# Optimization experiments

Measured on AMD Instinct MI355X. Metric: run time of the kernel, lower is better.

## Reference

```python
import jax, jax.numpy as jnp
import numpy as np
import math

B, L, D, P = 2, 2048, 256, 32
PI = math.pi


def _layernorm(x, g, b, eps=1e-5):
    m = x.mean(-1, keepdims=True)
    v = x.var(-1, keepdims=True)
    return (x - m) / jnp.sqrt(v + eps) * g + b


def setup_inputs() -> dict:
    key = jax.random.key(0)
    ks = jax.random.split(key, 16)
    sd = 1.0 / math.sqrt(D)
    f32 = jnp.float32
    inp = {
        "x": jax.random.normal(ks[0], (B, L, D), f32),
        # key_encoder: Linear(D, P)
        "key_W": jax.random.normal(ks[1], (D, P), f32) * sd,
        "key_b": jnp.zeros((P,), f32),
        # value_encoder: Linear(D, D)
        "val_W": jax.random.normal(ks[2], (D, D), f32) * sd,
        "val_b": jnp.zeros((D,), f32),
        # refiner: LayerNorm(D), Linear(D, 2D), GELU, Linear(2D, D)
        "ln1_g": jnp.ones((D,), f32),
        "ln1_b": jnp.zeros((D,), f32),
        "W1": jax.random.normal(ks[3], (D, 2 * D), f32) * sd,
        "b1": jnp.zeros((2 * D,), f32),
        "W2": jax.random.normal(ks[4], (2 * D, D), f32) * (1.0 / math.sqrt(2 * D)),
        "b2": jnp.zeros((D,), f32),
        # to_out: LayerNorm(D), Linear(D, D)
        "ln2_g": jnp.ones((D,), f32),
        "ln2_b": jnp.zeros((D,), f32),
        "Wo": jax.random.normal(ks[5], (D, D), f32) * sd,
        "bo": jnp.zeros((D,), f32),
    }
    return inp


def reference(x, key_W, key_b, val_W, val_b, ln1_g, ln1_b, W1, b1, W2, b2,
              ln2_g, ln2_b, Wo, bo):
    # key phases in (-pi, pi); phasor exp(i*theta) handled as (cos, sin)
    phases = jnp.tanh(x @ key_W + key_b) * PI          # (B, L, P)
    values = x @ val_W + val_b                          # (B, L, D)

    cos_p = jnp.cos(phases)
    sin_p = jnp.sin(phases)
    # torch.roll(shifts=1, dims=1) then zero the first position -> shift right, row 0 = 0
    zrow = jnp.zeros_like(cos_p[:, :1])
    cos_s = jnp.concatenate([zrow, cos_p[:, :-1]], axis=1)
    sin_s = jnp.concatenate([zrow, sin_p[:, :-1]], axis=1)

    # odd positions hold values
    vmask = (jnp.arange(L) % 2 == 1).astype(x.dtype)    # (L,)
    mv = values * vmask[None, :, None]                  # (B, L, D)

    # bind: outer product phasor (P) x value (D); real/imag parts
    bound_re = cos_s[..., None] * mv[:, :, None, :]     # (B, L, P, D)
    bound_im = sin_s[..., None] * mv[:, :, None, :]
    mem_re = jnp.cumsum(bound_re, axis=1)
    mem_im = jnp.cumsum(bound_im, axis=1)

    # retrieve: Re[ memory * exp(-i*theta) ] summed over phases
    retrieved = (jnp.einsum('blpd,blp->bld', mem_re, cos_p)
                 + jnp.einsum('blpd,blp->bld', mem_im, sin_p))

    valid = jnp.maximum(jnp.cumsum(vmask), 1.0)         # (L,)
    retrieved = retrieved / (jnp.sqrt(valid)[None, :, None] * math.sqrt(P))

    h = _layernorm(retrieved, ln1_g, ln1_b)
    h = jax.nn.gelu(h @ W1 + b1, approximate=False)
    refined = h @ W2 + b2
    out = x + (_layernorm(refined, ln2_g, ln2_b) @ Wo + bo)
    return out
```

## Files before the change

kernel.cpp:

```cpp
#include <hip/hip_runtime.h>
#include <math.h>

#define BB 2
#define LL 2048
#define DD 256
#define PP 32
#define NC 64
#define PI_F 3.14159265358979323846f

typedef __attribute__((ext_vector_type(8))) short bf16x8;
typedef __attribute__((ext_vector_type(4))) float f32x4;
typedef unsigned short ushort_t;
typedef unsigned int uint_t;

__device__ inline ushort_t f2bf(float x) {
    uint_t u = __float_as_uint(x);
    uint_t r = (u + 0x7fffu + ((u >> 16) & 1u)) >> 16;
    return (ushort_t)r;
}

__device__ inline int swzc(int row, int col) {
    return (col & ~63) | ((((col >> 3) & 7) ^ (row & 7)) << 3);
}
__device__ inline int swze(int row, int col) {
    return (col & ~63) | (col & 7) | ((((col >> 3) & 7) ^ (row & 7)) << 3);
}

__global__ __launch_bounds__(256) void prep_key_kernel(
    const float* __restrict__ W1, const float* __restrict__ W2,
    const float* __restrict__ Wo, const float* __restrict__ valW,
    const float* __restrict__ x, const float* __restrict__ key_W,
    const float* __restrict__ key_b,
    ushort_t* __restrict__ W1t, ushort_t* __restrict__ W2t,
    ushort_t* __restrict__ Wot, ushort_t* __restrict__ valWt,
    float2* __restrict__ ph)
{
    const int bid = blockIdx.x;
    const int t = threadIdx.x;
    if (bid < 96) {
        __shared__ float T[64][65];
        const float* W; ushort_t* Wt; int K, N, tile;
        if (bid < 32)      { W = W1;   Wt = W1t;   K = 256; N = 512; tile = bid; }
        else if (bid < 64) { W = W2;   Wt = W2t;   K = 512; N = 256; tile = bid - 32; }
        else if (bid < 80) { W = Wo;   Wt = Wot;   K = 256; N = 256; tile = bid - 64; }
        else               { W = valW; Wt = valWt; K = 256; N = 256; tile = bid - 80; }
        const int ntiles = N / 64;
        const int k0 = (tile / ntiles) * 64, n0 = (tile % ntiles) * 64;
        {
            const int rr = t >> 2, cb = (t & 3) * 16;
            #pragma unroll
            for (int i = 0; i < 16; i += 4) {
                const float4 v = *(const float4*)&W[(k0 + rr) * N + n0 + cb + i];
                T[rr][cb + i + 0] = v.x; T[rr][cb + i + 1] = v.y;
                T[rr][cb + i + 2] = v.z; T[rr][cb + i + 3] = v.w;
            }
        }
        __syncthreads();
        {
            const int n = t >> 2, kb = (t & 3) * 16;
            #pragma unroll
            for (int i = 0; i < 16; ++i)
                Wt[(n0 + n) * K + k0 + kb + i] = f2bf(T[kb + i][n]);
        }
    } else {
        __shared__ ushort_t xt[16][264];
        __shared__ ushort_t kwT[32][264];
        __shared__ float rbuf[4][2][16][17];
        const int row0 = (bid - 96) * 16;
        {
            const int l = t >> 4, cb = (t & 15) * 16;
            const float* src = &x[(long)(row0 + l) * DD + cb];
            ushort_t tmp[16];
            #pragma unroll
            for (int i = 0; i < 4; ++i) {
                const float4 v = *(const float4*)&src[i * 4];
                tmp[i*4+0] = f2bf(v.x); tmp[i*4+1] = f2bf(v.y);
                tmp[i*4+2] = f2bf(v.z); tmp[i*4+3] = f2bf(v.w);
            }
            *(uint4*)&xt[l][cb]     = *(uint4*)&tmp[0];
            *(uint4*)&xt[l][cb + 8] = *(uint4*)&tmp[8];
        }
        {
            #pragma unroll
            for (int i = 0; i < 8; ++i) {
                const int idx4 = i * 256 + t;
                const int k = idx4 >> 3, pc = (idx4 & 7) * 4;
                const float4 v = *(const float4*)&key_W[k * 32 + pc];
                kwT[pc + 0][k] = f2bf(v.x);
                kwT[pc + 1][k] = f2bf(v.y);
                kwT[pc + 2][k] = f2bf(v.z);
                kwT[pc + 3][k] = f2bf(v.w);
            }
        }
        __syncthreads();
        const int wv = t >> 6, lane = t & 63;
        const int qd = lane >> 4, mc = lane & 15;
        f32x4 acc0 = {0.f,0.f,0.f,0.f}, acc1 = {0.f,0.f,0.f,0.f};
        #pragma unroll
        for (int ks = 0; ks < 2; ++ks) {
            const int ko = wv * 64 + ks * 32 + qd * 8;
            const bf16x8 a  = *(const bf16x8*)&xt[mc][ko];
            const bf16x8 b0 = *(const bf16x8*)&kwT[mc][ko];
            const bf16x8 b1 = *(const bf16x8*)&kwT[16 + mc][ko];
            acc0 = __builtin_amdgcn_mfma_f32_16x16x32_bf16(a, b0, acc0, 0, 0, 0);
            acc1 = __builtin_amdgcn_mfma_f32_16x16x32_bf16(a, b1, acc1, 0, 0, 0);
        }
        #pragma unroll
        for (int r = 0; r < 4; ++r) {
            rbuf[wv][0][qd * 4 + r][mc] = acc0[r];
            rbuf[wv][1][qd * 4 + r][mc] = acc1[r];
        }
        __syncthreads();
        #pragma unroll
        for (int rep = 0; rep < 2; ++rep) {
            const int idx = rep * 256 + t;
            const int p = idx & 31, l = idx >> 5;
            const int nf = p >> 4, mcol = p & 15;
            float a = key_b[p] + rbuf[0][nf][l][mcol] + rbuf[1][nf][l][mcol]
                    + rbuf[2][nf][l][mcol] + rbuf[3][nf][l][mcol];
            a = tanhf(a) * PI_F;
            float sn, cs;
            sincosf(a, &sn, &cs);
            ph[(long)(row0 + l) * PP + p] = make_float2(cs, sn);
        }
    }
}

__global__ __launch_bounds__(256) void valbind_kernel(
    const float* __restrict__ x, const float2* __restrict__ ph,
    const ushort_t* __restrict__ valWt, const float* __restrict__ val_b,
    ushort_t* __restrict__ VoddT, float* __restrict__ Mt)
{
    __shared__ ushort_t xsb[16][264];
    __shared__ ushort_t VdT[64][40];
    __shared__ ushort_t phsT[64][40];
    __shared__ float    Ms[64][68];

    const int tid = threadIdx.x;
    const int bid = blockIdx.x;
    const int b  = bid >> 8;
    const int c  = (bid >> 2) & 63;
    const int dq = bid & 3;
    const int base = b * LL;
    const int r0 = 32 * c;

    {
        const int j = tid >> 4, cb = (tid & 15) * 16;
        const float* src = &x[(long)(base + r0 + 2 * j + 1) * DD + cb];
        ushort_t tmp[16];
        #pragma unroll
        for (int i = 0; i < 4; ++i) {
            const float4 v = *(const float4*)&src[i * 4];
            tmp[i*4+0] = f2bf(v.x); tmp[i*4+1] = f2bf(v.y);
            tmp[i*4+2] = f2bf(v.z); tmp[i*4+3] = f2bf(v.w);
        }
        *(uint4*)&xsb[j][cb]     = *(uint4*)&tmp[0];
        *(uint4*)&xsb[j][cb + 8] = *(uint4*)&tmp[8];
    }
    {
        const int j = tid >> 4, qb = (tid & 15) * 4;
        const float4 v = *(const float4*)((const float*)ph +
                              (long)(base + r0 + 2 * j) * 64 + qb);
        phsT[qb + 0][j] = f2bf(v.x);
        phsT[qb + 1][j] = f2bf(v.y);
        phsT[qb + 2][j] = f2bf(v.z);
        phsT[qb + 3][j] = f2bf(v.w);
    }
    for (int e = tid; e < 64 * 16; e += 256) {
        phsT[e >> 4][16 + (e & 15)] = 0;
        VdT[e >> 4][16 + (e & 15)] = 0;
    }
    __syncthreads();

    const int wv = tid >> 6, lane = tid & 63;
    const int qd = lane >> 4, mc = lane & 15;

    f32x4 va = {0.f,0.f,0.f,0.f};
    const int dloc = wv * 16 + mc;
    const int ng = dq * 64 + dloc;
    const ushort_t* B0 = &valWt[(long)ng * 256];
    #pragma unroll
    for (int ks = 0; ks < 8; ++ks) {
        const bf16x8 a  = *(const bf16x8*)&xsb[mc][ks * 32 + qd * 8];
        const bf16x8 b0 = *(const bf16x8*)&B0[ks * 32 + qd * 8];
        va = __builtin_amdgcn_mfma_f32_16x16x32_bf16(a, b0, va, 0, 0, 0);
    }
    {
        const float bb = val_b[ng];
        #pragma unroll
        for (int r = 0; r < 4; ++r)
            VdT[dloc][qd * 4 + r] = f2bf(va[r] + bb);
    }
    __syncthreads();

    const bf16x8 a2 = *(const bf16x8*)&phsT[wv * 16 + mc][qd * 8];
    f32x4 macc[4];
    #pragma unroll
    for (int nf = 0; nf < 4; ++nf) {
        f32x4 z = {0.f,0.f,0.f,0.f};
        const bf16x8 b2 = *(const bf16x8*)&VdT[nf * 16 + mc][qd * 8];
        macc[nf] = __builtin_amdgcn_mfma_f32_16x16x32_bf16(a2, b2, z, 0, 0, 0);
    }
    #pragma unroll
    for (int nf = 0; nf < 4; ++nf) {
        #pragma unroll
        for (int r = 0; r < 4; ++r)
            Ms[nf * 16 + mc][wv * 16 + qd * 4 + r] = macc[nf][r];
    }
    __syncthreads();

    {
        float* dst = &Mt[((long)(b * NC + c) * 256 + dq * 64) * 64];
        #pragma unroll
        for (int p = 0; p < 4; ++p) {
            const int idx4 = p * 256 + tid;
            const int dl = idx4 >> 4, q4 = (idx4 & 15) * 4;
            *(float4*)&dst[dl * 64 + q4] = *(const float4*)&Ms[dl][q4];
        }
    }
    if (tid < 64) {
        ushort_t* vd = &VoddT[((long)(b * NC + c) * 256 + dq * 64 + tid) * 16];
        *(uint4*)&vd[0] = *(const uint4*)&VdT[tid][0];
        *(uint4*)&vd[8] = *(const uint4*)&VdT[tid][8];
    }
}

__global__ __launch_bounds__(256) void prefix_kernel(
    const float* __restrict__ M, ushort_t* __restrict__ Mpre_b)
{
    __shared__ float segsum[4][64];
    const int tid = threadIdx.x;
    const int b  = blockIdx.x >> 8;
    const int cg = blockIdx.x & 255;
    const int col = cg * 64 + (tid & 63);
    const int seg = tid >> 6;
    const long base = (long)b * NC * 16384 + col;

    float v[16], s = 0.f;
    #pragma unroll
    for (int i = 0; i < 16; ++i) {
        v[i] = M[base + (long)(seg * 16 + i) * 16384];
        s += v[i];
    }
    segsum[seg][tid & 63] = s;
    __syncthreads();
    float run = 0.f;
    #pragma unroll
    for (int sg = 0; sg < 3; ++sg)
        if (sg < seg) run += segsum[sg][tid & 63];
    #pragma unroll
    for (int i = 0; i < 16; ++i) {
        const long a = base + (long)(seg * 16 + i) * 16384;
        Mpre_b[a] = f2bf(run);
        run += v[i];
    }
}

__global__ __launch_bounds__(512) void retrieve_mlp_kernel(
    const float* __restrict__ ph, const ushort_t* __restrict__ Mpre_b,
    const ushort_t* __restrict__ VoddT,
    const float* __restrict__ ln1_g, const float* __restrict__ ln1_b,
    const ushort_t* __restrict__ W1t, const float* __restrict__ b1,
    const ushort_t* __restrict__ W2t, const float* __restrict__ b2,
    const float* __restrict__ ln2_g, const float* __restrict__ ln2_b,
    const ushort_t* __restrict__ Wot, const float* __restrict__ bo,
    const float* __restrict__ x, float* __restrict__ out)
{
    __shared__ ushort_t Bs_v[256][32];
    __shared__ ushort_t As_ph[16][64];
    __shared__ ushort_t Bs_sh[16][64];
    __shared__ ushort_t As_p[16][40];
    __shared__ float    refct[16][264];
    __shared__ ushort_t rhat_s[16][256];
    __shared__ ushort_t h_s[16][512];
    __shared__ ushort_t shT[16][256];

    const int tid = threadIdx.x;
    const int b = blockIdx.x >> 7;
    const int c = (blockIdx.x >> 1) & 63;
    const int h = blockIdx.x & 1;
    const int l0g = 32 * c + 16 * h;
    const long rowbase = (long)b * LL + l0g;

    if (tid < 256) {
        const int r = tid >> 4, q4 = (tid & 15) * 4;
        const int c4 = swze(r, q4);
        const float4 vv = *(const float4*)((const float*)ph + (rowbase + r) * 64 + q4);
        ushort_t t0[4] = {f2bf(vv.x), f2bf(vv.y), f2bf(vv.z), f2bf(vv.w)};
        *(uint2*)&As_ph[r][c4] = *(uint2*)t0;
        const float4 w = *(const float4*)((const float*)ph +
                             ((long)b * LL + 32 * c + 2 * r) * 64 + q4);
        ushort_t t1[4] = {f2bf(w.x), f2bf(w.y), f2bf(w.z), f2bf(w.w)};
        *(uint2*)&Bs_sh[r][c4] = *(uint2*)t1;
    }
    {
        const ushort_t* src = &VoddT[(long)(b * NC + c) * 4096];
        const int rw = tid >> 1, cch = tid & 1;
        *(uint4*)&Bs_v[rw][8 * (cch ^ (rw & 3))] = *(const uint4*)&src[tid * 8];
        *(uint4*)&Bs_v[rw][8 * ((2 + cch) ^ (rw & 3))] = make_uint4(0, 0, 0, 0);
        if (tid < 256) As_p[tid >> 4][16 + (tid & 15)] = 0;
    }
    __syncthreads();

    const int wv = tid >> 6, lane = tid & 63;
    const int qd = lane >> 4, mc = lane & 15;
    const int m7 = mc & 7;

    {
        f32x4 sacc = {0.f, 0.f, 0.f, 0.f};
        #pragma unroll
        for (int ks = 0; ks < 2; ++ks) {
            const int lc = 8 * ((ks * 4 + qd) ^ m7);
            const bf16x8 a  = *(const bf16x8*)&As_ph[mc][lc];
            const bf16x8 bb = *(const bf16x8*)&Bs_sh[mc][lc];
            sacc = __builtin_amdgcn_mfma_f32_16x16x32_bf16(a, bb, sacc, 0, 0, 0);
        }
        if (wv == 0) {
            #pragma unroll
            for (int r = 0; r < 4; ++r) {
                const int l = qd * 4 + r;
                As_p[l][mc] = (2 * mc + 1 <= 16 * h + l) ? f2bf(sacc[r])
                                                         : (ushort_t)0;
            }
        }
    }

    const ushort_t* msrc = &Mpre_b[(long)(b * NC + c) * 16384];
    f32x4 acc[2];
    #pragma unroll
    for (int i = 0; i < 2; ++i) acc[i] = (f32x4){0.f, 0.f, 0.f, 0.f};
    #pragma unroll
    for (int i = 0; i < 2; ++i) {
        const int d0 = wv * 32 + i * 16;
        #pragma unroll
        for (int ks = 0; ks < 2; ++ks) {
            const int lc = 8 * ((ks * 4 + qd) ^ m7);
            const bf16x8 a  = *(const bf16x8*)&As_ph[mc][lc];
            const bf16x8 bb = *(const bf16x8*)&msrc[(long)(d0 + mc) * 64 + ks * 32 + qd * 8];
            acc[i] = __builtin_amdgcn_mfma_f32_16x16x32_bf16(a, bb, acc[i], 0, 0, 0);
        }
    }
    __syncthreads();

    {
        const bf16x8 a2 = *(const bf16x8*)&As_p[mc][qd * 8];
        #pragma unroll
        for (int i = 0; i < 2; ++i) {
            const int d0 = wv * 32 + i * 16;
            const bf16x8 b2 = *(const bf16x8*)&Bs_v[d0 + mc][8 * (qd ^ (mc & 3))];
            acc[i] = __builtin_amdgcn_mfma_f32_16x16x32_bf16(a2, b2, acc[i], 0, 0, 0);
        }
    }

    #pragma unroll
    for (int r = 0; r < 4; ++r) {
        const int l = qd * 4 + r;
        int va = (l0g + l + 1) >> 1; if (va < 1) va = 1;
        const float sc = 0.17677669529663687f * rsqrtf((float)va);
        #pragma unroll
        for (int i = 0; i < 2; ++i)
            refct[l][wv * 32 + i * 16 + mc] = acc[i][r] * sc;
    }
    __syncthreads();

    {
        const int row = tid >> 5, cg = (tid & 31) * 8;
        float s = 0.f, sq = 0.f;
        #pragma unroll
        for (int i = 0; i < 8; ++i) {
            const float v = refct[row][cg + i];
            s += v; sq += v * v;
        }
        s += __shfl_xor(s, 1, 32);  sq += __shfl_xor(sq, 1, 32);
        s += __shfl_xor(s, 2, 32);  sq += __shfl_xor(sq, 2, 32);
        s += __shfl_xor(s, 4, 32);  sq += __shfl_xor(sq, 4, 32);
        s += __shfl_xor(s, 8, 32);  sq += __shfl_xor(sq, 8, 32);
        s += __shfl_xor(s, 16, 32); sq += __shfl_xor(sq, 16, 32);
        const float m = s * (1.f / 256.f);
        const float inv = rsqrtf(sq * (1.f / 256.f) - m * m + 1e-5f);
        ushort_t o16[8];
        #pragma unroll
        for (int i = 0; i < 8; ++i) {
            const int cc = cg + i;
            o16[i] = f2bf((refct[row][cc] - m) * inv * ln1_g[cc] + ln1_b[cc]);
        }
        *(uint4*)&rhat_s[row][swzc(row, cg)] = *(uint4*)&o16[0];
    }
    __syncthreads();

    #pragma unroll
    for (int nh = 0; nh < 2; ++nh) {
        f32x4 acc1[2];
        acc1[0] = (f32x4){0.f,0.f,0.f,0.f};
        acc1[1] = (f32x4){0.f,0.f,0.f,0.f};
        const long nb0 = (long)(nh * 256 + wv * 32 + mc) * 256;
        const long nb1 = (long)(nh * 256 + wv * 32 + 16 + mc) * 256;
        #pragma unroll
        for (int k0 = 0; k0 < 256; k0 += 64) {
            #pragma unroll
            for (int ks = 0; ks < 2; ++ks) {
                const int kk = k0 + ks * 32 + qd * 8;
                const int lc = 8 * ((ks * 4 + qd) ^ m7);
                const bf16x8 a  = *(const bf16x8*)&rhat_s[mc][k0 + lc];
                const bf16x8 b0 = *(const bf16x8*)&W1t[nb0 + kk];
                const bf16x8 b1v = *(const bf16x8*)&W1t[nb1 + kk];
                acc1[0] = __builtin_amdgcn_mfma_f32_16x16x32_bf16(a, b0, acc1[0], 0, 0, 0);
                acc1[1] = __builtin_amdgcn_mfma_f32_16x16x32_bf16(a, b1v, acc1[1], 0, 0, 0);
            }
        }
        #pragma unroll
        for (int nf = 0; nf < 2; ++nf) {
            const int n = nh * 256 + wv * 32 + nf * 16 + mc;
            const float bb = b1[n];
            #pragma unroll
            for (int r = 0; r < 4; ++r) {
                float v = acc1[nf][r] + bb;
                v = 0.5f * v * (1.f + erff(v * 0.70710678118654752f));
                const int rw = qd * 4 + r;
                h_s[rw][swze(rw, n)] = f2bf(v);
            }
        }
    }
    __syncthreads();

    f32x4 acc2[2];
    acc2[0] = (f32x4){0.f,0.f,0.f,0.f};
    acc2[1] = (f32x4){0.f,0.f,0.f,0.f};
    {
        const long nb0 = (long)(wv * 32 + mc) * 512;
        const long nb1 = (long)(wv * 32 + 16 + mc) * 512;
        #pragma unroll
        for (int k0 = 0; k0 < 512; k0 += 64) {
            #pragma unroll
            for (int ks = 0; ks < 2; ++ks) {
                const int kk = k0 + ks * 32 + qd * 8;
                const int lc = 8 * ((ks * 4 + qd) ^ m7);
                const bf16x8 a  = *(const bf16x8*)&h_s[mc][k0 + lc];
                const bf16x8 b0 = *(const bf16x8*)&W2t[nb0 + kk];
                const bf16x8 b1v = *(const bf16x8*)&W2t[nb1 + kk];
                acc2[0] = __builtin_amdgcn_mfma_f32_16x16x32_bf16(a, b0, acc2[0], 0, 0, 0);
                acc2[1] = __builtin_amdgcn_mfma_f32_16x16x32_bf16(a, b1v, acc2[1], 0, 0, 0);
            }
        }
    }
    #pragma unroll
    for (int nf = 0; nf < 2; ++nf) {
        const int n = wv * 32 + nf * 16 + mc;
        const float bb = b2[n];
        #pragma unroll
        for (int r = 0; r < 4; ++r)
            refct[qd * 4 + r][n] = acc2[nf][r] + bb;
    }
    __syncthreads();

    {
        const int row = tid >> 5, cg = (tid & 31) * 8;
        float s = 0.f, sq = 0.f;
        #pragma unroll
        for (int i = 0; i < 8; ++i) {
            const float v = refct[row][cg + i];
            s += v; sq += v * v;
        }
        s += __shfl_xor(s, 1, 32);  sq += __shfl_xor(sq, 1, 32);
        s += __shfl_xor(s, 2, 32);  sq += __shfl_xor(sq, 2, 32);
        s += __shfl_xor(s, 4, 32);  sq += __shfl_xor(sq, 4, 32);
        s += __shfl_xor(s, 8, 32);  sq += __shfl_xor(sq, 8, 32);
        s += __shfl_xor(s, 16, 32); sq += __shfl_xor(sq, 16, 32);
        const float m = s * (1.f / 256.f);
        const float inv = rsqrtf(sq * (1.f / 256.f) - m * m + 1e-5f);
        ushort_t o16[8];
        #pragma unroll
        for (int i = 0; i < 8; ++i) {
            const int cc = cg + i;
            o16[i] = f2bf((refct[row][cc] - m) * inv * ln2_g[cc] + ln2_b[cc]);
        }
        *(uint4*)&shT[row][swzc(row, cg)] = *(uint4*)&o16[0];
    }
    __syncthreads();

    f32x4 acc3[2];
    acc3[0] = (f32x4){0.f,0.f,0.f,0.f};
    acc3[1] = (f32x4){0.f,0.f,0.f,0.f};
    {
        const long nb0 = (long)(wv * 32 + mc) * 256;
        const long nb1 = (long)(wv * 32 + 16 + mc) * 256;
        #pragma unroll
        for (int k0 = 0; k0 < 256; k0 += 64) {
            #pragma unroll
            for (int ks = 0; ks < 2; ++ks) {
                const int kk = k0 + ks * 32 + qd * 8;
                const int lc = 8 * ((ks * 4 + qd) ^ m7);
                const bf16x8 a  = *(const bf16x8*)&shT[mc][k0 + lc];
                const bf16x8 b0 = *(const bf16x8*)&Wot[nb0 + kk];
                const bf16x8 b1v = *(const bf16x8*)&Wot[nb1 + kk];
                acc3[0] = __builtin_amdgcn_mfma_f32_16x16x32_bf16(a, b0, acc3[0], 0, 0, 0);
                acc3[1] = __builtin_amdgcn_mfma_f32_16x16x32_bf16(a, b1v, acc3[1], 0, 0, 0);
            }
        }
    }
    #pragma unroll
    for (int nf = 0; nf < 2; ++nf) {
        const int n = wv * 32 + nf * 16 + mc;
        const float bb = bo[n];
        #pragma unroll
        for (int r = 0; r < 4; ++r) {
            const long row = rowbase + qd * 4 + r;
            out[row * DD + n] = acc3[nf][r] + bb + x[row * DD + n];
        }
    }
}

extern "C" void kernel_launch(void* const* d_in, const int* in_sizes, int n_in,
                              void* d_out, int out_size, void* d_ws, size_t ws_size,
                              hipStream_t stream)
{
    const float* x     = (const float*)d_in[0];
    const float* key_W = (const float*)d_in[1];
    const float* key_b = (const float*)d_in[2];
    const float* val_W = (const float*)d_in[3];
    const float* val_b = (const float*)d_in[4];
    const float* ln1_g = (const float*)d_in[5];
    const float* ln1_b = (const float*)d_in[6];
    const float* W1    = (const float*)d_in[7];
    const float* b1    = (const float*)d_in[8];
    const float* W2    = (const float*)d_in[9];
    const float* b2    = (const float*)d_in[10];
    const float* ln2_g = (const float*)d_in[11];
    const float* ln2_b = (const float*)d_in[12];
    const float* Wo    = (const float*)d_in[13];
    const float* bo    = (const float*)d_in[14];
    float* outp = (float*)d_out;

    float* ws = (float*)d_ws;
    float*  ph      = ws;
    float*  Mt      = ws + 262144;
    ushort_t* Mpre_b = (ushort_t*)(Mt + 2097152);
    ushort_t* VoddT  = Mpre_b + 2097152;
    ushort_t* rhat_b = VoddT + 524288;
    ushort_t* W1t   = rhat_b + 1048576;
    ushort_t* W2t   = W1t + 131072;
    ushort_t* Wot   = W2t + 131072;
    ushort_t* valWt = Wot + 65536;

    prep_key_kernel<<<352, 256, 0, stream>>>(W1, W2, Wo, val_W, x, key_W, key_b,
                                             W1t, W2t, Wot, valWt, (float2*)ph);
    valbind_kernel<<<512, 256, 0, stream>>>(x, (const float2*)ph, valWt, val_b,
                                            VoddT, Mt);
    prefix_kernel<<<512, 256, 0, stream>>>(Mt, Mpre_b);
    retrieve_mlp_kernel<<<256, 512, 0, stream>>>(ph, Mpre_b, VoddT, ln1_g, ln1_b,
                                                 W1t, b1, W2t, b2, ln2_g, ln2_b,
                                                 Wot, bo, x, outp);
}
```

Baseline: 124.2 us.

## Double block to 1024 threads and stage weight tiles through LDS

The retrieve/MLP kernel now runs 16 waves per block, and each wave computes one 16-column tile instead of two. The memory prefix tile and the W1/W2/Wo weight slices are loaded cooperatively into a swizzled shared buffer, replacing per-wave direct global fragment loads. This aims to coalesce weight reads and raise the number of waves in flight. In exchange it adds two block-wide barriers per K-step, and with a 16-row M tile the weights are reused little, so the barriers may dominate.

```diff
diff --git a/kernel.cpp b/kernel.cpp
--- a/kernel.cpp
+++ b/kernel.cpp
@@ -256,7 +256,7 @@
     }
 }
 
-__global__ __launch_bounds__(512) void retrieve_mlp_kernel(
+__global__ __launch_bounds__(1024) void retrieve_mlp_kernel(
     const float* __restrict__ ph, const ushort_t* __restrict__ Mpre_b,
     const ushort_t* __restrict__ VoddT,
     const float* __restrict__ ln1_g, const float* __restrict__ ln1_b,
@@ -266,6 +266,7 @@
     const ushort_t* __restrict__ Wot, const float* __restrict__ bo,
     const float* __restrict__ x, float* __restrict__ out)
 {
+    __shared__ ushort_t Bs_m[256][64];
     __shared__ ushort_t Bs_v[256][32];
     __shared__ ushort_t As_ph[16][64];
     __shared__ ushort_t Bs_sh[16][64];
@@ -282,6 +283,15 @@
     const int l0g = 32 * c + 16 * h;
     const long rowbase = (long)b * LL + l0g;
 
+    {
+        const ushort_t* src = &Mpre_b[(long)(b * NC + c) * 16384];
+        #pragma unroll
+        for (int p = 0; p < 2; ++p) {
+            const int idx8 = p * 1024 + tid;
+            const int d = idx8 >> 3, ch = idx8 & 7;
+            *(uint4*)&Bs_m[d][8 * (ch ^ (d & 7))] = *(const uint4*)&src[idx8 * 8];
+        }
+    }
     if (tid < 256) {
         const int r = tid >> 4, q4 = (tid & 15) * 4;
         const int c4 = swze(r, q4);
@@ -293,18 +303,22 @@
         ushort_t t1[4] = {f2bf(w.x), f2bf(w.y), f2bf(w.z), f2bf(w.w)};
         *(uint2*)&Bs_sh[r][c4] = *(uint2*)t1;
     }
-    {
+    if (tid < 512) {
         const ushort_t* src = &VoddT[(long)(b * NC + c) * 4096];
         const int rw = tid >> 1, cch = tid & 1;
         *(uint4*)&Bs_v[rw][8 * (cch ^ (rw & 3))] = *(const uint4*)&src[tid * 8];
         *(uint4*)&Bs_v[rw][8 * ((2 + cch) ^ (rw & 3))] = make_uint4(0, 0, 0, 0);
-        if (tid < 256) As_p[tid >> 4][16 + (tid & 15)] = 0;
+    }
+    if (tid >= 512 && tid < 768) {
+        const int e = tid - 512;
+        As_p[e >> 4][16 + (e & 15)] = 0;
     }
     __syncthreads();
 
     const int wv = tid >> 6, lane = tid & 63;
     const int qd = lane >> 4, mc = lane & 15;
     const int m7 = mc & 7;
+    const int d0 = wv * 16;
 
     {
         f32x4 sacc = {0.f, 0.f, 0.f, 0.f};
@@ -325,31 +339,20 @@
         }
     }
 
-    const ushort_t* msrc = &Mpre_b[(long)(b * NC + c) * 16384];
-    f32x4 acc[2];
-    #pragma unroll
-    for (int i = 0; i < 2; ++i) acc[i] = (f32x4){0.f, 0.f, 0.f, 0.f};
-    #pragma unroll
-    for (int i = 0; i < 2; ++i) {
-        const int d0 = wv * 32 + i * 16;
-        #pragma unroll
-        for (int ks = 0; ks < 2; ++ks) {
-            const int lc = 8 * ((ks * 4 + qd) ^ m7);
-            const bf16x8 a  = *(const bf16x8*)&As_ph[mc][lc];
-            const bf16x8 bb = *(const bf16x8*)&msrc[(long)(d0 + mc) * 64 + ks * 32 + qd * 8];
-            acc[i] = __builtin_amdgcn_mfma_f32_16x16x32_bf16(a, bb, acc[i], 0, 0, 0);
-        }
+    f32x4 acc = {0.f, 0.f, 0.f, 0.f};
+    #pragma unroll
+    for (int ks = 0; ks < 2; ++ks) {
+        const int lc = 8 * ((ks * 4 + qd) ^ m7);
+        const bf16x8 a  = *(const bf16x8*)&As_ph[mc][lc];
+        const bf16x8 bb = *(const bf16x8*)&Bs_m[d0 + mc][lc];
+        acc = __builtin_amdgcn_mfma_f32_16x16x32_bf16(a, bb, acc, 0, 0, 0);
     }
     __syncthreads();
 
     {
         const bf16x8 a2 = *(const bf16x8*)&As_p[mc][qd * 8];
-        #pragma unroll
-        for (int i = 0; i < 2; ++i) {
-            const int d0 = wv * 32 + i * 16;
-            const bf16x8 b2 = *(const bf16x8*)&Bs_v[d0 + mc][8 * (qd ^ (mc & 3))];
-            acc[i] = __builtin_amdgcn_mfma_f32_16x16x32_bf16(a2, b2, acc[i], 0, 0, 0);
-        }
+        const bf16x8 b2 = *(const bf16x8*)&Bs_v[d0 + mc][8 * (qd ^ (mc & 3))];
+        acc = __builtin_amdgcn_mfma_f32_16x16x32_bf16(a2, b2, acc, 0, 0, 0);
     }
 
     #pragma unroll
@@ -357,64 +360,63 @@
         const int l = qd * 4 + r;
         int va = (l0g + l + 1) >> 1; if (va < 1) va = 1;
         const float sc = 0.17677669529663687f * rsqrtf((float)va);
-        #pragma unroll
-        for (int i = 0; i < 2; ++i)
-            refct[l][wv * 32 + i * 16 + mc] = acc[i][r] * sc;
-    }
-    __syncthreads();
-
-    {
-        const int row = tid >> 5, cg = (tid & 31) * 8;
+        refct[l][d0 + mc] = acc[r] * sc;
+    }
+    __syncthreads();
+
+    {
+        const int row = tid >> 6, cg = (tid & 63) * 4;
         float s = 0.f, sq = 0.f;
         #pragma unroll
-        for (int i = 0; i < 8; ++i) {
+        for (int i = 0; i < 4; ++i) {
             const float v = refct[row][cg + i];
             s += v; sq += v * v;
         }
-        s += __shfl_xor(s, 1, 32);  sq += __shfl_xor(sq, 1, 32);
-        s += __shfl_xor(s, 2, 32);  sq += __shfl_xor(sq, 2, 32);
-        s += __shfl_xor(s, 4, 32);  sq += __shfl_xor(sq, 4, 32);
-        s += __shfl_xor(s, 8, 32);  sq += __shfl_xor(sq, 8, 32);
-        s += __shfl_xor(s, 16, 32); sq += __shfl_xor(sq, 16, 32);
+        s += __shfl_xor(s, 1, 64);  sq += __shfl_xor(sq, 1, 64);
+        s += __shfl_xor(s, 2, 64);  sq += __shfl_xor(sq, 2, 64);
+        s += __shfl_xor(s, 4, 64);  sq += __shfl_xor(sq, 4, 64);
+        s += __shfl_xor(s, 8, 64);  sq += __shfl_xor(sq, 8, 64);
+        s += __shfl_xor(s, 16, 64); sq += __shfl_xor(sq, 16, 64);
+        s += __shfl_xor(s, 32, 64); sq += __shfl_xor(sq, 32, 64);
         const float m = s * (1.f / 256.f);
         const float inv = rsqrtf(sq * (1.f / 256.f) - m * m + 1e-5f);
-        ushort_t o16[8];
-        #pragma unroll
-        for (int i = 0; i < 8; ++i) {
+        ushort_t o4[4];
+        #pragma unroll
+        for (int i = 0; i < 4; ++i) {
             const int cc = cg + i;
-            o16[i] = f2bf((refct[row][cc] - m) * inv * ln1_g[cc] + ln1_b[cc]);
-        }
-        *(uint4*)&rhat_s[row][swzc(row, cg)] = *(uint4*)&o16[0];
+            o4[i] = f2bf((refct[row][cc] - m) * inv * ln1_g[cc] + ln1_b[cc]);
+        }
+        *(uint2*)&rhat_s[row][swze(row, cg)] = *(uint2*)&o4[0];
     }
     __syncthreads();
 
     #pragma unroll
     for (int nh = 0; nh < 2; ++nh) {
-        f32x4 acc1[2];
-        acc1[0] = (f32x4){0.f,0.f,0.f,0.f};
-        acc1[1] = (f32x4){0.f,0.f,0.f,0.f};
-        const long nb0 = (long)(nh * 256 + wv * 32 + mc) * 256;
-        const long nb1 = (long)(nh * 256 + wv * 32 + 16 + mc) * 256;
-        #pragma unroll
+        f32x4 acc1 = {0.f,0.f,0.f,0.f};
         for (int k0 = 0; k0 < 256; k0 += 64) {
+            __syncthreads();
+            #pragma unroll
+            for (int p = 0; p < 2; ++p) {
+                const int idx8 = p * 1024 + tid;
+                const int d = idx8 >> 3, ch = idx8 & 7;
+                *(uint4*)&Bs_m[d][8 * (ch ^ (d & 7))] =
+                    *(const uint4*)&W1t[(long)(nh * 256 + d) * 256 + k0 + ch * 8];
+            }
+            __syncthreads();
             #pragma unroll
             for (int ks = 0; ks < 2; ++ks) {
-                const int kk = k0 + ks * 32 + qd * 8;
                 const int lc = 8 * ((ks * 4 + qd) ^ m7);
                 const bf16x8 a  = *(const bf16x8*)&rhat_s[mc][k0 + lc];
-                const bf16x8 b0 = *(const bf16x8*)&W1t[nb0 + kk];
-                const bf16x8 b1v = *(const bf16x8*)&W1t[nb1 + kk];
-                acc1[0] = __builtin_amdgcn_mfma_f32_16x16x32_bf16(a, b0, acc1[0], 0, 0, 0);
-                acc1[1] = __builtin_amdgcn_mfma_f32_16x16x32_bf16(a, b1v, acc1[1], 0, 0, 0);
-            }
-        }
-        #pragma unroll
-        for (int nf = 0; nf < 2; ++nf) {
-            const int n = nh * 256 + wv * 32 + nf * 16 + mc;
+                const bf16x8 bb = *(const bf16x8*)&Bs_m[d0 + mc][lc];
+                acc1 = __builtin_amdgcn_mfma_f32_16x16x32_bf16(a, bb, acc1, 0, 0, 0);
+            }
+        }
+        {
+            const int n = nh * 256 + d0 + mc;
             const float bb = b1[n];
             #pragma unroll
             for (int r = 0; r < 4; ++r) {
-                float v = acc1[nf][r] + bb;
+                float v = acc1[r] + bb;
                 v = 0.5f * v * (1.f + erff(v * 0.70710678118654752f));
                 const int rw = qd * 4 + r;
                 h_s[rw][swze(rw, n)] = f2bf(v);
@@ -423,89 +425,86 @@
     }
     __syncthreads();
 
-    f32x4 acc2[2];
-    acc2[0] = (f32x4){0.f,0.f,0.f,0.f};
-    acc2[1] = (f32x4){0.f,0.f,0.f,0.f};
-    {
-        const long nb0 = (long)(wv * 32 + mc) * 512;
-        const long nb1 = (long)(wv * 32 + 16 + mc) * 512;
-        #pragma unroll
-        for (int k0 = 0; k0 < 512; k0 += 64) {
-            #pragma unroll
-            for (int ks = 0; ks < 2; ++ks) {
-                const int kk = k0 + ks * 32 + qd * 8;
-                const int lc = 8 * ((ks * 4 + qd) ^ m7);
-                const bf16x8 a  = *(const bf16x8*)&h_s[mc][k0 + lc];
-                const bf16x8 b0 = *(const bf16x8*)&W2t[nb0 + kk];
-                const bf16x8 b1v = *(const bf16x8*)&W2t[nb1 + kk];
-                acc2[0] = __builtin_amdgcn_mfma_f32_16x16x32_bf16(a, b0, acc2[0], 0, 0, 0);
-                acc2[1] = __builtin_amdgcn_mfma_f32_16x16x32_bf16(a, b1v, acc2[1], 0, 0, 0);
-            }
-        }
-    }
-    #pragma unroll
-    for (int nf = 0; nf < 2; ++nf) {
-        const int n = wv * 32 + nf * 16 + mc;
+    f32x4 acc2 = {0.f,0.f,0.f,0.f};
+    for (int k0 = 0; k0 < 512; k0 += 64) {
+        __syncthreads();
+        #pragma unroll
+        for (int p = 0; p < 2; ++p) {
+            const int idx8 = p * 1024 + tid;
+            const int d = idx8 >> 3, ch = idx8 & 7;
+            *(uint4*)&Bs_m[d][8 * (ch ^ (d & 7))] =
+                *(const uint4*)&W2t[(long)d * 512 + k0 + ch * 8];
+        }
+        __syncthreads();
+        #pragma unroll
+        for (int ks = 0; ks < 2; ++ks) {
+            const int lc = 8 * ((ks * 4 + qd) ^ m7);
+            const bf16x8 a  = *(const bf16x8*)&h_s[mc][k0 + lc];
+            const bf16x8 bb = *(const bf16x8*)&Bs_m[d0 + mc][lc];
+            acc2 = __builtin_amdgcn_mfma_f32_16x16x32_bf16(a, bb, acc2, 0, 0, 0);
+        }
+    }
+    {
+        const int n = d0 + mc;
         const float bb = b2[n];
         #pragma unroll
         for (int r = 0; r < 4; ++r)
-            refct[qd * 4 + r][n] = acc2[nf][r] + bb;
-    }
-    __syncthreads();
-
-    {
-        const int row = tid >> 5, cg = (tid & 31) * 8;
+            refct[qd * 4 + r][n] = acc2[r] + bb;
+    }
+    __syncthreads();
+
+    {
+        const int row = tid >> 6, cg = (tid & 63) * 4;
         float s = 0.f, sq = 0.f;
         #pragma unroll
-        for (int i = 0; i < 8; ++i) {
+        for (int i = 0; i < 4; ++i) {
             const float v = refct[row][cg + i];
             s += v; sq += v * v;
         }
-        s += __shfl_xor(s, 1, 32);  sq += __shfl_xor(sq, 1, 32);
-        s += __shfl_xor(s, 2, 32);  sq += __shfl_xor(sq, 2, 32);
-        s += __shfl_xor(s, 4, 32);  sq += __shfl_xor(sq, 4, 32);
-        s += __shfl_xor(s, 8, 32);  sq += __shfl_xor(sq, 8, 32);
-        s += __shfl_xor(s, 16, 32); sq += __shfl_xor(sq, 16, 32);
+        s += __shfl_xor(s, 1, 64);  sq += __shfl_xor(sq, 1, 64);
+        s += __shfl_xor(s, 2, 64);  sq += __shfl_xor(sq, 2, 64);
+        s += __shfl_xor(s, 4, 64);  sq += __shfl_xor(sq, 4, 64);
+        s += __shfl_xor(s, 8, 64);  sq += __shfl_xor(sq, 8, 64);
+        s += __shfl_xor(s, 16, 64); sq += __shfl_xor(sq, 16, 64);
+        s += __shfl_xor(s, 32, 64); sq += __shfl_xor(sq, 32, 64);
         const float m = s * (1.f / 256.f);
         const float inv = rsqrtf(sq * (1.f / 256.f) - m * m + 1e-5f);
-        ushort_t o16[8];
-        #pragma unroll
-        for (int i = 0; i < 8; ++i) {
+        ushort_t o4[4];
+        #pragma unroll
+        for (int i = 0; i < 4; ++i) {
             const int cc = cg + i;
-            o16[i] = f2bf((refct[row][cc] - m) * inv * ln2_g[cc] + ln2_b[cc]);
-        }
-        *(uint4*)&shT[row][swzc(row, cg)] = *(uint4*)&o16[0];
-    }
-    __syncthreads();
-
-    f32x4 acc3[2];
-    acc3[0] = (f32x4){0.f,0.f,0.f,0.f};
-    acc3[1] = (f32x4){0.f,0.f,0.f,0.f};
-    {
-        const long nb0 = (long)(wv * 32 + mc) * 256;
-        const long nb1 = (long)(wv * 32 + 16 + mc) * 256;
-        #pragma unroll
-        for (int k0 = 0; k0 < 256; k0 += 64) {
-            #pragma unroll
-            for (int ks = 0; ks < 2; ++ks) {
-                const int kk = k0 + ks * 32 + qd * 8;
-                const int lc = 8 * ((ks * 4 + qd) ^ m7);
-                const bf16x8 a  = *(const bf16x8*)&shT[mc][k0 + lc];
-                const bf16x8 b0 = *(const bf16x8*)&Wot[nb0 + kk];
-                const bf16x8 b1v = *(const bf16x8*)&Wot[nb1 + kk];
-                acc3[0] = __builtin_amdgcn_mfma_f32_16x16x32_bf16(a, b0, acc3[0], 0, 0, 0);
-                acc3[1] = __builtin_amdgcn_mfma_f32_16x16x32_bf16(a, b1v, acc3[1], 0, 0, 0);
-            }
-        }
-    }
-    #pragma unroll
-    for (int nf = 0; nf < 2; ++nf) {
-        const int n = wv * 32 + nf * 16 + mc;
+            o4[i] = f2bf((refct[row][cc] - m) * inv * ln2_g[cc] + ln2_b[cc]);
+        }
+        *(uint2*)&shT[row][swze(row, cg)] = *(uint2*)&o4[0];
+    }
+    __syncthreads();
+
+    f32x4 acc3 = {0.f,0.f,0.f,0.f};
+    for (int k0 = 0; k0 < 256; k0 += 64) {
+        __syncthreads();
+        #pragma unroll
+        for (int p = 0; p < 2; ++p) {
+            const int idx8 = p * 1024 + tid;
+            const int d = idx8 >> 3, ch = idx8 & 7;
+            *(uint4*)&Bs_m[d][8 * (ch ^ (d & 7))] =
+                *(const uint4*)&Wot[(long)d * 256 + k0 + ch * 8];
+        }
+        __syncthreads();
+        #pragma unroll
+        for (int ks = 0; ks < 2; ++ks) {
+            const int lc = 8 * ((ks * 4 + qd) ^ m7);
+            const bf16x8 a  = *(const bf16x8*)&shT[mc][k0 + lc];
+            const bf16x8 bb = *(const bf16x8*)&Bs_m[d0 + mc][lc];
+            acc3 = __builtin_amdgcn_mfma_f32_16x16x32_bf16(a, bb, acc3, 0, 0, 0);
+        }
+    }
+    {
+        const int n = d0 + mc;
         const float bb = bo[n];
         #pragma unroll
         for (int r = 0; r < 4; ++r) {
             const long row = rowbase + qd * 4 + r;
-            out[row * DD + n] = acc3[nf][r] + bb + x[row * DD + n];
+            out[row * DD + n] = acc3[r] + bb + x[row * DD + n];
         }
     }
 }
@@ -547,7 +546,7 @@
     valbind_kernel<<<512, 256, 0, stream>>>(x, (const float2*)ph, valWt, val_b,
                                             VoddT, Mt);
     prefix_kernel<<<512, 256, 0, stream>>>(Mt, Mpre_b);
-    retrieve_mlp_kernel<<<256, 512, 0, stream>>>(ph, Mpre_b, VoddT, ln1_g, ln1_b,
-                                                 W1t, b1, W2t, b2, ln2_g, ln2_b,
-                                                 Wot, bo, x, outp);
-}
+    retrieve_mlp_kernel<<<256, 1024, 0, stream>>>(ph, Mpre_b, VoddT, ln1_g, ln1_b,
+                                                  W1t, b1, W2t, b2, ln2_g, ln2_b,
+                                                  Wot, bo, x, outp);
+}
```

New measurement: 123.0 us. About the same (-1.0%).
